# Kernel tuning notes

Measured on AMD Instinct MI355X. Metric: run time of the kernel, lower is better.

Reference implementation:

```python
import jax, jax.numpy as jnp
import numpy as np

B, D_IN, H, NZ, NC = 32768, 768, 2048, 128, 1024
EPS, NITERS = 0.5, 15


def setup_inputs() -> dict:
    key = jax.random.key(0)
    ks = jax.random.split(key, 4)
    x = jax.random.normal(ks[0], (B, D_IN), jnp.float32)
    # scaled init so feature magnitudes keep exp(-dist/eps) in f32 range
    W1 = jax.random.normal(ks[1], (D_IN, H), jnp.float32) / np.sqrt(D_IN)
    b1 = jnp.zeros((H,), jnp.float32)
    W2 = jax.random.normal(ks[2], (H, NZ), jnp.float32) / np.sqrt(H)
    b2 = jnp.zeros((NZ,), jnp.float32)
    centroids = jax.random.normal(ks[3], (NC, NZ), jnp.float32)
    return {
        'x': x, 'W1': W1, 'b1': b1, 'W2': W2, 'b2': b2,
        'centroids': centroids,
        'cluster_counts': jnp.zeros((NC,), jnp.int32),
        'raw_counts': jnp.zeros((NC,), jnp.int32),
        'total_soft_counts': jnp.zeros((NC,), jnp.float32),
    }


def _sinkhorn(scores, eps=EPS, niters=NITERS):
    # scores: [B, K].  Q: [K, B], matches torch reference where sum(Q) = col-sums.
    Q = jnp.exp(scores / eps).T
    Q = Q / jnp.sum(Q, axis=0, keepdims=True)
    K, Bb = Q.shape
    r = 1.0 / K
    c = 1.0 / Bb

    def body(Q, _):
        Q = Q * (r / jnp.sum(Q, axis=1))[:, None]
        Q = Q * (c / jnp.sum(Q, axis=0))[None, :]
        return Q, None

    Q, _ = jax.lax.scan(body, Q, None, length=niters)
    return (Q / jnp.sum(Q, axis=0, keepdims=True)).T  # [B, K]


def reference(x, W1, b1, W2, b2, centroids, cluster_counts, raw_counts, total_soft_counts):
    # fc backbone: Linear -> ReLU -> Linear
    fv = jax.nn.relu(x @ W1 + b1) @ W2 + b2                        # [B, nz]
    # pairwise euclidean distances to centroids (cdist via gram trick;
    # avoids materializing the [B, nc, nz] broadcast torch creates)
    sq = (jnp.sum(fv * fv, axis=1)[:, None]
          + jnp.sum(centroids * centroids, axis=1)[None, :]
          - 2.0 * fv @ centroids.T)
    cluster_dists = jnp.sqrt(jnp.maximum(sq, 1e-12))               # [B, nc]

    # sinkhorn branch (no_grad in torch)
    soft_assignments = jax.lax.stop_gradient(_sinkhorn(-cluster_dists))
    batch_assignments = jnp.argmin(soft_assignments, axis=1)       # [B]
    soft_counts = jnp.sum(soft_assignments, axis=0)                # [nc]
    # soft_train=False: gather assigned distances
    loss = jnp.mean(jnp.take_along_axis(cluster_dists, batch_assignments[:, None], axis=1))

    # scatter-accumulate counts
    new_raw = raw_counts.at[jnp.argmin(cluster_dists, axis=1)].add(1)
    new_cluster = cluster_counts.at[batch_assignments].add(1)
    new_total_soft = total_soft_counts + soft_counts
    return loss, batch_assignments, soft_counts, new_raw, new_cluster, new_total_soft
```

## Files before the change

kernel.cpp:

```cpp
#include <hip/hip_runtime.h>
#include <math.h>

#define BN    32768
#define DIN   768
#define HN    2048
#define NZ    128
#define NCN   1024

typedef __attribute__((ext_vector_type(8))) short s16x8;
typedef __attribute__((ext_vector_type(4))) float f32x4;
typedef unsigned short u16;

#define MFMA16(a,b,c) __builtin_amdgcn_mfma_f32_16x16x32_bf16(a,b,c,0,0,0)

__device__ __forceinline__ u16 bf16_rne(float x){
  unsigned u = __float_as_uint(x);
  unsigned r = (u + 0x7FFFu + ((u >> 16) & 1u)) >> 16;
  return (u16)r;
}
__device__ __forceinline__ float bf16_tof(u16 h){
  return __uint_as_float(((unsigned)h) << 16);
}
__device__ __forceinline__ void split3(float x, u16& h, u16& m, u16& l){
  h = bf16_rne(x);
  float r1 = x - bf16_tof(h);
  m = bf16_rne(r1);
  float r2 = r1 - bf16_tof(m);
  l = bf16_rne(r2);
}

__device__ __forceinline__ void gload16(const void* gsrc, void* lds){
  __builtin_amdgcn_global_load_lds(
      (const __attribute__((address_space(1))) unsigned int*)gsrc,
      (__attribute__((address_space(3))) unsigned int*)lds, 16, 0, 0);
}

__global__ __launch_bounds__(1024) void k0_init(float* u, int* hraw, int* hclu){
  const int k = threadIdx.x;
  u[k] = 1.0f;
  hraw[k] = 0;
  hclu[k] = 0;
}

__global__ __launch_bounds__(256) void c_tsplit(
    const float* __restrict__ in, int R, int C,
    u16* __restrict__ oh, u16* __restrict__ om, u16* __restrict__ ol)
{
  __shared__ float L[64][65];
  const int t = threadIdx.x;
  const int bi = blockIdx.x, bj = blockIdx.y;
  #pragma unroll
  for (int m=0;m<4;++m){
    int flat = t + 256*m;
    int r = flat >> 4, c4 = (flat & 15) << 2;
    const float4 v = *(const float4*)&in[(size_t)(bi*64 + r)*C + bj*64 + c4];
    L[r][c4+0] = v.x; L[r][c4+1] = v.y; L[r][c4+2] = v.z; L[r][c4+3] = v.w;
  }
  __syncthreads();
  #pragma unroll
  for (int m=0;m<4;++m){
    int flat = t + 256*m;
    int oc = flat >> 4, k4 = (flat & 15) << 2;
    ushort4 h4, m4, l4;
    split3(L[k4+0][oc], h4.x, m4.x, l4.x);
    split3(L[k4+1][oc], h4.y, m4.y, l4.y);
    split3(L[k4+2][oc], h4.z, m4.z, l4.z);
    split3(L[k4+3][oc], h4.w, m4.w, l4.w);
    size_t off = (size_t)(bj*64 + oc)*R + bi*64 + k4;
    *(ushort4*)&oh[off] = h4;
    *(ushort4*)&om[off] = m4;
    *(ushort4*)&ol[off] = l4;
  }
}

__global__ __launch_bounds__(256, 2) void k1_mfma(
    const float* __restrict__ X,
    const u16* __restrict__ W1h, const u16* __restrict__ W1m, const u16* __restrict__ W1l,
    const float* __restrict__ b1,
    const u16* __restrict__ W2h, const u16* __restrict__ W2m, const u16* __restrict__ W2l,
    const float* __restrict__ b2, float* __restrict__ fv)
{
  __shared__ __align__(16) unsigned char sm[73728];
  unsigned char* xsr = sm;
  unsigned char* wsr = sm + 24576;

  const int t  = threadIdx.x;
  const int l  = t & 63;
  const int wn = t >> 6;
  const int g  = (l >> 4) & 3;
  const int lr = l & 15;
  const int row0 = blockIdx.x * 64;

  f32x4 fvacc[4][2];
  #pragma unroll
  for (int mf=0;mf<4;++mf){
    fvacc[mf][0] = (f32x4){0.f,0.f,0.f,0.f};
    fvacc[mf][1] = (f32x4){0.f,0.f,0.f,0.f};
  }

  #pragma unroll 1
  for (int nc = 0; nc < 16; ++nc){
    f32x4 a1acc[4][2];
    #pragma unroll
    for (int mf=0;mf<4;++mf){
      a1acc[mf][0] = (f32x4){0.f,0.f,0.f,0.f};
      a1acc[mf][1] = (f32x4){0.f,0.f,0.f,0.f};
    }

    #pragma unroll 1
    for (int ks = 0; ks < 12; ++ks){
      #pragma unroll
      for (int m=0;m<4;++m){
        const int flat = t + 256*m;
        const int xr = flat >> 4;
        const int c4 = (flat & 15) << 2;
        f32x4 v = *(const f32x4*)&X[(size_t)(row0+xr)*768 + ks*64 + c4];
        ushort4 h4, m4, l4;
        split3(v[0], h4.x, m4.x, l4.x);
        split3(v[1], h4.y, m4.y, l4.y);
        split3(v[2], h4.z, m4.z, l4.z);
        split3(v[3], h4.w, m4.w, l4.w);
        const int bo = xr*128 + ((2*c4) ^ ((xr & 7) << 4));
        *(ushort4*)(xsr + bo)          = h4;
        *(ushort4*)(xsr + 8192 + bo)   = m4;
        *(ushort4*)(xsr + 16384 + bo)  = l4;
      }
      #pragma unroll
      for (int i=0;i<12;++i){
        const int ci = wn*12 + i;
        const int s  = ci >> 4;
        const int rb = ci & 15;
        const int rloc = rb*8 + (l >> 3);
        const int q  = l & 7;
        const u16* Wp = (s==0) ? W1h : ((s==1) ? W1m : W1l);
        const u16* src = Wp + (size_t)(nc*128 + rloc)*768 + ks*64 + ((q ^ (rloc & 7)) << 3);
        gload16(src, wsr + s*16384 + rb*1024);
      }
      __syncthreads();

      #pragma unroll
      for (int kk=0;kk<2;++kk){
        s16x8 Bf[3][2], Af[3][4];
        #pragma unroll
        for (int s=0;s<3;++s){
          #pragma unroll
          for (int nf=0;nf<2;++nf){
            const int br = wn*32 + nf*16 + lr;
            Bf[s][nf] = *(const s16x8*)(wsr + s*16384 + br*128 + ((16*(g + 4*kk)) ^ ((br & 7) << 4)));
          }
          #pragma unroll
          for (int mf=0;mf<4;++mf){
            const int ar = mf*16 + lr;
            Af[s][mf] = *(const s16x8*)(xsr + s*8192 + ar*128 + ((16*(g + 4*kk)) ^ ((ar & 7) << 4)));
          }
        }
        #pragma unroll
        for (int mf=0;mf<4;++mf){
          #pragma unroll
          for (int nf=0;nf<2;++nf){
            f32x4 acc = a1acc[mf][nf];
            acc = MFMA16(Af[0][mf], Bf[0][nf], acc);
            acc = MFMA16(Af[0][mf], Bf[1][nf], acc);
            acc = MFMA16(Af[1][mf], Bf[0][nf], acc);
            acc = MFMA16(Af[1][mf], Bf[1][nf], acc);
            acc = MFMA16(Af[0][mf], Bf[2][nf], acc);
            acc = MFMA16(Af[2][mf], Bf[0][nf], acc);
            a1acc[mf][nf] = acc;
          }
        }
      }
      __syncthreads();
    }

    const float b1v0 = b1[nc*128 + wn*32 + lr];
    const float b1v1 = b1[nc*128 + wn*32 + 16 + lr];

    #pragma unroll
    for (int half=0; half<2; ++half){
      if ((wn >> 1) == half){
        #pragma unroll
        for (int mf=0;mf<4;++mf){
          #pragma unroll
          for (int nf=0;nf<2;++nf){
            const int klocal = (wn & 1)*32 + nf*16 + lr;
            #pragma unroll
            for (int r=0;r<4;++r){
              float vv = a1acc[mf][nf][r] + ((nf==0) ? b1v0 : b1v1);
              vv = vv > 0.f ? vv : 0.f;
              u16 sh, sm2, sl;
              split3(vv, sh, sm2, sl);
              const int ar = mf*16 + g*4 + r;
              const int bo = ar*128 + ((2*klocal) ^ ((ar & 7) << 4));
              *(u16*)(xsr + bo)         = sh;
              *(u16*)(xsr + 8192 + bo)  = sm2;
              *(u16*)(xsr + 16384 + bo) = sl;
            }
          }
        }
      }
      #pragma unroll
      for (int i=0;i<12;++i){
        const int ci = wn*12 + i;
        const int s  = ci >> 4;
        const int rb = ci & 15;
        const int rloc = rb*8 + (l >> 3);
        const int q  = l & 7;
        const u16* Wp = (s==0) ? W2h : ((s==1) ? W2m : W2l);
        const u16* src = Wp + (size_t)rloc*2048 + nc*128 + half*64 + ((q ^ (rloc & 7)) << 3);
        gload16(src, wsr + s*16384 + rb*1024);
      }
      __syncthreads();

      #pragma unroll
      for (int kk=0;kk<2;++kk){
        s16x8 Bf[3][2], Af[3][4];
        #pragma unroll
        for (int s=0;s<3;++s){
          #pragma unroll
          for (int nf=0;nf<2;++nf){
            const int br = wn*32 + nf*16 + lr;
            Bf[s][nf] = *(const s16x8*)(wsr + s*16384 + br*128 + ((16*(g + 4*kk)) ^ ((br & 7) << 4)));
          }
          #pragma unroll
          for (int mf=0;mf<4;++mf){
            const int ar = mf*16 + lr;
            Af[s][mf] = *(const s16x8*)(xsr + s*8192 + ar*128 + ((16*(g + 4*kk)) ^ ((ar & 7) << 4)));
          }
        }
        #pragma unroll
        for (int mf=0;mf<4;++mf){
          #pragma unroll
          for (int nf=0;nf<2;++nf){
            f32x4 acc = fvacc[mf][nf];
            acc = MFMA16(Af[0][mf], Bf[0][nf], acc);
            acc = MFMA16(Af[0][mf], Bf[1][nf], acc);
            acc = MFMA16(Af[1][mf], Bf[0][nf], acc);
            acc = MFMA16(Af[1][mf], Bf[1][nf], acc);
            acc = MFMA16(Af[0][mf], Bf[2][nf], acc);
            acc = MFMA16(Af[2][mf], Bf[0][nf], acc);
            fvacc[mf][nf] = acc;
          }
        }
      }
      __syncthreads();
    }
  }

  const float b2v0 = b2[wn*32 + lr];
  const float b2v1 = b2[wn*32 + 16 + lr];
  #pragma unroll
  for (int mf=0;mf<4;++mf){
    #pragma unroll
    for (int nf=0;nf<2;++nf){
      #pragma unroll
      for (int r=0;r<4;++r){
        const int frow = row0 + mf*16 + g*4 + r;
        const int col  = wn*32 + nf*16 + lr;
        fv[(size_t)frow*NZ + col] = fvacc[mf][nf][r] + ((nf==0) ? b2v0 : b2v1);
      }
    }
  }
}

__global__ __launch_bounds__(256) void k2_dist(
    const float* __restrict__ fv, const float* __restrict__ cent,
    float* __restrict__ Q0)
{
  __shared__ __align__(16) float fvs[32*128];
  __shared__ __align__(16) float cs[64*128];
  __shared__ float fvn[32];
  __shared__ float cn[64];
  const int t = threadIdx.x;
  const int tx = t & 15, ty = t >> 4;
  const int row0 = blockIdx.x * 32;

  #pragma unroll
  for (int m=0;m<4;++m){
    int idx4 = t + 256*m;
    int r  = idx4 >> 5;
    int c4 = (idx4 & 31) << 2;
    *(float4*)&fvs[r*128 + (c4 ^ ((((r>>1)&7))<<2))] =
        *(const float4*)&fv[(size_t)(row0 + r)*NZ + c4];
  }
  __syncthreads();
  if (t < 32){
    int xw = ((t>>1)&7)<<2;
    float s = 0.f;
    for (int z=0;z<NZ;z+=4){
      const float4 v = *(const float4*)&fvs[t*128 + (z ^ xw)];
      s += v.x*v.x; s += v.y*v.y; s += v.z*v.z; s += v.w*v.w;
    }
    fvn[t] = s;
  }

  for (int cc = 0; cc < NCN; cc += 64){
    #pragma unroll
    for (int m=0;m<8;++m){
      int idx4 = t + 256*m;
      int r  = idx4 >> 5;
      int c4 = (idx4 & 31) << 2;
      *(float4*)&cs[r*128 + (c4 ^ ((((r>>3)&7))<<2))] =
          *(const float4*)&cent[(size_t)(cc + r)*NZ + c4];
    }
    __syncthreads();
    if (t < 64){
      int xw = ((t>>3)&7)<<2;
      float s = 0.f;
      for (int z=0;z<NZ;z+=4){
        const float4 v = *(const float4*)&cs[t*128 + (z ^ xw)];
        s += v.x*v.x; s += v.y*v.y; s += v.z*v.z; s += v.w*v.w;
      }
      cn[t] = s;
    }
    __syncthreads();

    float acc[2][4];
    #pragma unroll
    for (int i=0;i<2;++i)
      #pragma unroll
      for (int j=0;j<4;++j) acc[i][j]=0.f;

    const int xwf = (ty&7)<<2;
    const int xwc = ((tx>>1)&7)<<2;
    #pragma unroll 4
    for (int kk=0; kk<NZ; kk+=4){
      float4 fq0 = *(const float4*)&fvs[(2*ty+0)*128 + (kk ^ xwf)];
      float4 fq1 = *(const float4*)&fvs[(2*ty+1)*128 + (kk ^ xwf)];
      float4 cb[4];
      #pragma unroll
      for (int j=0;j<4;++j)
        cb[j] = *(const float4*)&cs[(4*tx+j)*128 + (kk ^ xwc)];
      #pragma unroll
      for (int j=0;j<4;++j){
        acc[0][j] += fq0.x*cb[j].x; acc[0][j] += fq0.y*cb[j].y;
        acc[0][j] += fq0.z*cb[j].z; acc[0][j] += fq0.w*cb[j].w;
        acc[1][j] += fq1.x*cb[j].x; acc[1][j] += fq1.y*cb[j].y;
        acc[1][j] += fq1.z*cb[j].z; acc[1][j] += fq1.w*cb[j].w;
      }
    }
    #pragma unroll
    for (int i=0;i<2;++i){
      int row = row0 + 2*ty + i;
      float fnv = fvn[2*ty+i];
      float o[4];
      #pragma unroll
      for (int j=0;j<4;++j){
        float sq = fnv + cn[4*tx+j] - 2.0f*acc[i][j];
        sq = sq > 1e-12f ? sq : 1e-12f;
        float d = sqrtf(sq);
        o[j] = expf(-2.0f*d);
      }
      float4 ov; ov.x=o[0]; ov.y=o[1]; ov.z=o[2]; ov.w=o[3];
      *(float4*)&Q0[(size_t)row*NCN + cc + 4*tx] = ov;
    }
    __syncthreads();
  }
}

__global__ __launch_bounds__(256) void k3_pass(
    const float* __restrict__ Q0, const float* __restrict__ u,
    float* __restrict__ S_part, float alpha)
{
  __shared__ __align__(16) float ul[NCN];
  __shared__ __align__(16) float Sw[4][NCN];
  const int t = threadIdx.x;
  const int w = t >> 6, l = t & 63;
  #pragma unroll
  for (int m=0;m<4;++m) ul[t + 256*m] = u[t + 256*m];
  #pragma unroll
  for (int m=0;m<16;++m) (&Sw[0][0])[t + 256*m] = 0.f;
  __syncthreads();

  const float4* ul4 = (const float4*)ul;
  float4* Sw4 = (float4*)&Sw[w][0];
  const int gw = blockIdx.x*4 + w;
  const size_t b0 = (size_t)gw * 16;
  for (int rr=0; rr<16; ++rr){
    const float4* qrow = (const float4*)(Q0 + (b0 + rr)*NCN);
    float4 q4[4];
    float part = 0.f;
    #pragma unroll
    for (int j=0;j<4;++j){
      q4[j] = qrow[l + 64*j];
      float4 uu = ul4[l + 64*j];
      part += q4[j].x*uu.x; part += q4[j].y*uu.y;
      part += q4[j].z*uu.z; part += q4[j].w*uu.w;
    }
    #pragma unroll
    for (int off=32; off; off>>=1) part += __shfl_xor(part, off, 64);
    const float v = alpha / part;
    #pragma unroll
    for (int j=0;j<4;++j){
      float4 s = Sw4[l + 64*j];
      s.x += q4[j].x*v; s.y += q4[j].y*v; s.z += q4[j].z*v; s.w += q4[j].w*v;
      Sw4[l + 64*j] = s;
    }
  }
  __syncthreads();
  #pragma unroll
  for (int m=0;m<4;++m){
    int k = t + 256*m;
    S_part[(size_t)blockIdx.x*NCN + k] = ((Sw[0][k]+Sw[1][k])+(Sw[2][k]+Sw[3][k]));
  }
}

__global__ __launch_bounds__(256) void k4_unew(
    const float* __restrict__ S_part, float* __restrict__ u)
{
  __shared__ float P[4][64];
  const int t = threadIdx.x;
  const int col = blockIdx.x*64 + (t & 63);
  const int s4 = t >> 6;
  float p = 0.f;
  for (int i=0;i<128;++i)
    p += S_part[(size_t)(s4*128 + i)*NCN + col];
  P[s4][t & 63] = p;
  __syncthreads();
  if (s4 == 0){
    float tot = ((P[0][t] + P[1][t]) + (P[2][t] + P[3][t]));
    u[col] = (1.0f/1024.0f) / tot;
  }
}

__device__ __forceinline__ float comp4(const float4 v, int c){
  return (c==0)?v.x:(c==1)?v.y:(c==2)?v.z:v.w;
}

__global__ __launch_bounds__(256) void k5_final(
    const float* __restrict__ Q0, const float* __restrict__ u,
    float* __restrict__ softc_part, float* __restrict__ loss_part,
    int* __restrict__ hist_raw, int* __restrict__ hist_clu,
    float* __restrict__ out_ba)
{
  __shared__ __align__(16) float ul[NCN];
  __shared__ __align__(16) float Sw[4][NCN];
  __shared__ float lossw[4];
  const int t = threadIdx.x;
  const int w = t >> 6, l = t & 63;
  #pragma unroll
  for (int m=0;m<4;++m) ul[t + 256*m] = u[t + 256*m];
  #pragma unroll
  for (int m=0;m<16;++m) (&Sw[0][0])[t + 256*m] = 0.f;
  __syncthreads();

  const float4* ul4 = (const float4*)ul;
  float4* Sw4 = (float4*)&Sw[w][0];
  const int gw = blockIdx.x*4 + w;
  const size_t b0 = (size_t)gw * 32;
  float lacc = 0.f;
  for (int rr=0; rr<32; ++rr){
    const size_t b = b0 + rr;
    const float4* qrow = (const float4*)(Q0 + b*NCN);
    float4 q4[4], wv4[4];
    float part = 0.f;
    #pragma unroll
    for (int j=0;j<4;++j){
      q4[j] = qrow[l + 64*j];
      float4 uu = ul4[l + 64*j];
      wv4[j].x = uu.x*q4[j].x; wv4[j].y = uu.y*q4[j].y;
      wv4[j].z = uu.z*q4[j].z; wv4[j].w = uu.w*q4[j].w;
      part += wv4[j].x; part += wv4[j].y; part += wv4[j].z; part += wv4[j].w;
    }
    #pragma unroll
    for (int off=32; off; off>>=1) part += __shfl_xor(part, off, 64);
    const float inv = 1.0f / part;

    float smin = wv4[0].x * inv; int kmin = 4*l; float qat = q4[0].x;
    float qmax = q4[0].x;        int kmax = 4*l;
    #pragma unroll
    for (int j=0;j<4;++j){
      #pragma unroll
      for (int c=0;c<4;++c){
        if (j==0 && c==0) continue;
        float qv = comp4(q4[j], c);
        float sv = comp4(wv4[j], c) * inv;
        int k = 4*l + 256*j + c;
        if (sv < smin){ smin = sv; kmin = k; qat = qv; }
        if (qv > qmax){ qmax = qv; kmax = k; }
      }
    }
    #pragma unroll
    for (int off=32; off; off>>=1){
      float s2 = __shfl_xor(smin, off, 64);
      int   k2 = __shfl_xor(kmin, off, 64);
      float q2 = __shfl_xor(qat,  off, 64);
      if (s2 < smin || (s2 == smin && k2 < kmin)){ smin=s2; kmin=k2; qat=q2; }
      float m2 = __shfl_xor(qmax, off, 64);
      int   i2 = __shfl_xor(kmax, off, 64);
      if (m2 > qmax || (m2 == qmax && i2 < kmax)){ qmax=m2; kmax=i2; }
    }
    #pragma unroll
    for (int j=0;j<4;++j){
      float4 s = Sw4[l + 64*j];
      s.x += wv4[j].x*inv; s.y += wv4[j].y*inv;
      s.z += wv4[j].z*inv; s.w += wv4[j].w*inv;
      Sw4[l + 64*j] = s;
    }
    if (l == 0){
      out_ba[b] = (float)kmin;
      atomicAdd(&hist_clu[kmin], 1);
      atomicAdd(&hist_raw[kmax], 1);
      lacc += -0.5f * logf(qat);
    }
  }
  if (l == 0) lossw[w] = lacc;
  __syncthreads();
  #pragma unroll
  for (int m=0;m<4;++m){
    int k = t + 256*m;
    softc_part[(size_t)blockIdx.x*NCN + k] = ((Sw[0][k]+Sw[1][k])+(Sw[2][k]+Sw[3][k]));
  }
  if (t == 0) loss_part[blockIdx.x] = ((lossw[0]+lossw[1])+(lossw[2]+lossw[3]));
}

__global__ __launch_bounds__(1024) void k6_fin(
    const float* __restrict__ softc_part, const float* __restrict__ loss_part,
    const int* __restrict__ hist_raw, const int* __restrict__ hist_clu,
    const int* __restrict__ raw_in, const int* __restrict__ clu_in,
    const float* __restrict__ tsoft_in, float* __restrict__ out)
{
  const int k = threadIdx.x;
  float s0=0.f,s1=0.f,s2=0.f,s3=0.f;
  for (int blk=0; blk<256; blk+=4){
    s0 += softc_part[(size_t)(blk+0)*NCN + k];
    s1 += softc_part[(size_t)(blk+1)*NCN + k];
    s2 += softc_part[(size_t)(blk+2)*NCN + k];
    s3 += softc_part[(size_t)(blk+3)*NCN + k];
  }
  const float s = ((s0+s1)+(s2+s3));
  out[1 + BN + k]           = s;
  out[1 + BN + NCN + k]     = (float)(raw_in[k] + hist_raw[k]);
  out[1 + BN + 2*NCN + k]   = (float)(clu_in[k] + hist_clu[k]);
  out[1 + BN + 3*NCN + k]   = tsoft_in[k] + s;
  if (k == 0){
    float ls = 0.f;
    for (int i=0;i<256;++i) ls += loss_part[i];
    out[0] = ls / 32768.0f;
  }
}

extern "C" void kernel_launch(void* const* d_in, const int* in_sizes, int n_in,
                              void* d_out, int out_size, void* d_ws, size_t ws_size,
                              hipStream_t stream) {
  (void)in_sizes; (void)n_in; (void)out_size; (void)ws_size;
  const float* x      = (const float*)d_in[0];
  const float* W1     = (const float*)d_in[1];
  const float* b1     = (const float*)d_in[2];
  const float* W2     = (const float*)d_in[3];
  const float* b2     = (const float*)d_in[4];
  const float* cent   = (const float*)d_in[5];
  const int*   clu_in = (const int*)d_in[6];
  const int*   raw_in = (const int*)d_in[7];
  const float* tsoft  = (const float*)d_in[8];
  float* out = (float*)d_out;

  float* ws        = (float*)d_ws;
  float* fv        = ws;
  float* Q0        = ws + 4194304;
  float* u         = Q0 + 33554432;
  float* S_part    = u + 1024;
  float* softc_par = S_part + 524288;
  float* loss_par  = softc_par + 262144;
  int*   hist_raw  = (int*)(loss_par + 256);
  int*   hist_clu  = hist_raw + 1024;
  u16* W1Th = (u16*)(ws + 38538496);
  u16* W1Tm = W1Th + 1572864;
  u16* W1Tl = W1Tm + 1572864;
  u16* W2Th = W1Tl + 1572864;
  u16* W2Tm = W2Th + 262144;
  u16* W2Tl = W2Tm + 262144;

  c_tsplit<<<dim3(12, 32), 256, 0, stream>>>(W1, 768, 2048, W1Th, W1Tm, W1Tl);
  c_tsplit<<<dim3(32, 2),  256, 0, stream>>>(W2, 2048, 128, W2Th, W2Tm, W2Tl);
  k0_init<<<1, 1024, 0, stream>>>(u, hist_raw, hist_clu);
  k1_mfma<<<512, 256, 0, stream>>>(x, W1Th, W1Tm, W1Tl, b1, W2Th, W2Tm, W2Tl, b2, fv);
  k2_dist<<<1024, 256, 0, stream>>>(fv, cent, Q0);
  for (int it = 0; it < 15; ++it){
    const float alpha = (it == 0) ? 1.0f : (1.0f/32768.0f);
    k3_pass<<<512, 256, 0, stream>>>(Q0, u, S_part, alpha);
    k4_unew<<<16, 256, 0, stream>>>(S_part, u);
  }
  k5_final<<<256, 256, 0, stream>>>(Q0, u, softc_par, loss_par,
                                    hist_raw, hist_clu, out + 1);
  k6_fin<<<1, 1024, 0, stream>>>(softc_par, loss_par, hist_raw, hist_clu,
                                 raw_in, clu_in, tsoft, out);
}
```

Baseline: 1.451 ms.

## Presplit X into bf16 triples and move distance GEMM to split-bf16 MFMA

Input X is split once into three bf16 planes by a separate kernel, so k1 loads its A tiles directly into LDS with global_load_lds instead of re-splitting X in every one of its 16 N-chunks. The fp32 FMA distance kernel is replaced by a 6-term split-bf16 MFMA kernel, with fv and centroid norms precomputed by separate small kernels. This removes redundant conversion work and the scalar-FMA bottleneck, but adds extra HBM traffic for the split X (three u16 planes written then read) and several extra launches. Workspace buffers are aliased (X planes share Q0's space, fv and centroid planes share the weight planes' space).

```diff
diff --git a/kernel.cpp b/kernel.cpp
--- a/kernel.cpp
+++ b/kernel.cpp
@@ -40,6 +40,23 @@
   u[k] = 1.0f;
   hraw[k] = 0;
   hclu[k] = 0;
+}
+
+__global__ __launch_bounds__(256) void c_split(
+    const float* __restrict__ in, u16* __restrict__ oh, u16* __restrict__ om,
+    u16* __restrict__ ol, int n4)
+{
+  const int i = blockIdx.x*256 + threadIdx.x;
+  if (i >= n4) return;
+  const f32x4 v = *(const f32x4*)&in[(size_t)i*4];
+  ushort4 h4, m4, l4;
+  split3(v[0], h4.x, m4.x, l4.x);
+  split3(v[1], h4.y, m4.y, l4.y);
+  split3(v[2], h4.z, m4.z, l4.z);
+  split3(v[3], h4.w, m4.w, l4.w);
+  *(ushort4*)&oh[(size_t)i*4] = h4;
+  *(ushort4*)&om[(size_t)i*4] = m4;
+  *(ushort4*)&ol[(size_t)i*4] = l4;
 }
 
 __global__ __launch_bounds__(256) void c_tsplit(
@@ -73,8 +90,20 @@
   }
 }
 
+__global__ __launch_bounds__(256) void c_norm(
+    const float* __restrict__ in, float* __restrict__ out)
+{
+  const int w = threadIdx.x >> 6, l = threadIdx.x & 63;
+  const int row = blockIdx.x*4 + w;
+  const float2 v = *(const float2*)&in[(size_t)row*128 + l*2];
+  float s = v.x*v.x + v.y*v.y;
+  #pragma unroll
+  for (int off=32; off; off>>=1) s += __shfl_xor(s, off, 64);
+  if (l == 0) out[row] = s;
+}
+
 __global__ __launch_bounds__(256, 2) void k1_mfma(
-    const float* __restrict__ X,
+    const u16* __restrict__ Xh, const u16* __restrict__ Xm, const u16* __restrict__ Xl,
     const u16* __restrict__ W1h, const u16* __restrict__ W1m, const u16* __restrict__ W1l,
     const float* __restrict__ b1,
     const u16* __restrict__ W2h, const u16* __restrict__ W2m, const u16* __restrict__ W2l,
@@ -110,20 +139,15 @@
     #pragma unroll 1
     for (int ks = 0; ks < 12; ++ks){
       #pragma unroll
-      for (int m=0;m<4;++m){
-        const int flat = t + 256*m;
-        const int xr = flat >> 4;
-        const int c4 = (flat & 15) << 2;
-        f32x4 v = *(const f32x4*)&X[(size_t)(row0+xr)*768 + ks*64 + c4];
-        ushort4 h4, m4, l4;
-        split3(v[0], h4.x, m4.x, l4.x);
-        split3(v[1], h4.y, m4.y, l4.y);
-        split3(v[2], h4.z, m4.z, l4.z);
-        split3(v[3], h4.w, m4.w, l4.w);
-        const int bo = xr*128 + ((2*c4) ^ ((xr & 7) << 4));
-        *(ushort4*)(xsr + bo)          = h4;
-        *(ushort4*)(xsr + 8192 + bo)   = m4;
-        *(ushort4*)(xsr + 16384 + bo)  = l4;
+      for (int i=0;i<6;++i){
+        const int ci = wn*6 + i;
+        const int s  = ci >> 3;
+        const int rb = ci & 7;
+        const int xr = rb*8 + (l >> 3);
+        const int q  = l & 7;
+        const u16* Xp = (s==0) ? Xh : ((s==1) ? Xm : Xl);
+        const u16* src = Xp + (size_t)(row0 + xr)*768 + ks*64 + ((q ^ (xr & 7)) << 3);
+        gload16(src, xsr + s*8192 + rb*1024);
       }
       #pragma unroll
       for (int i=0;i<12;++i){
@@ -262,96 +286,88 @@
   }
 }
 
-__global__ __launch_bounds__(256) void k2_dist(
-    const float* __restrict__ fv, const float* __restrict__ cent,
+__global__ __launch_bounds__(256, 2) void k2_mfma(
+    const u16* __restrict__ fvh, const u16* __restrict__ fvm, const u16* __restrict__ fvl,
+    const u16* __restrict__ ch,  const u16* __restrict__ cm,  const u16* __restrict__ cl,
+    const float* __restrict__ fvn, const float* __restrict__ cn,
     float* __restrict__ Q0)
 {
-  __shared__ __align__(16) float fvs[32*128];
-  __shared__ __align__(16) float cs[64*128];
-  __shared__ float fvn[32];
-  __shared__ float cn[64];
-  const int t = threadIdx.x;
-  const int tx = t & 15, ty = t >> 4;
-  const int row0 = blockIdx.x * 32;
-
-  #pragma unroll
-  for (int m=0;m<4;++m){
-    int idx4 = t + 256*m;
-    int r  = idx4 >> 5;
-    int c4 = (idx4 & 31) << 2;
-    *(float4*)&fvs[r*128 + (c4 ^ ((((r>>1)&7))<<2))] =
-        *(const float4*)&fv[(size_t)(row0 + r)*NZ + c4];
-  }
-  __syncthreads();
-  if (t < 32){
-    int xw = ((t>>1)&7)<<2;
-    float s = 0.f;
-    for (int z=0;z<NZ;z+=4){
-      const float4 v = *(const float4*)&fvs[t*128 + (z ^ xw)];
-      s += v.x*v.x; s += v.y*v.y; s += v.z*v.z; s += v.w*v.w;
-    }
-    fvn[t] = s;
-  }
-
+  __shared__ __align__(16) unsigned char bs[49152];
+  __shared__ float cnl[NCN];
+  const int t  = threadIdx.x;
+  const int l  = t & 63;
+  const int wn = t >> 6;
+  const int g  = (l >> 4) & 3;
+  const int lr = l & 15;
+  const int row0 = blockIdx.x * 64;
+  const int arow = row0 + wn*16 + lr;
+
+  s16x8 Af[3][4];
+  #pragma unroll
+  for (int kk=0;kk<4;++kk){
+    const size_t ao = (size_t)arow*128 + kk*32 + g*8;
+    Af[0][kk] = *(const s16x8*)&fvh[ao];
+    Af[1][kk] = *(const s16x8*)&fvm[ao];
+    Af[2][kk] = *(const s16x8*)&fvl[ao];
+  }
+  #pragma unroll
+  for (int m=0;m<4;++m) cnl[t + 256*m] = cn[t + 256*m];
+  const f32x4 fvnv = *(const f32x4*)&fvn[row0 + wn*16 + g*4];
+
+  #pragma unroll 1
   for (int cc = 0; cc < NCN; cc += 64){
     #pragma unroll
-    for (int m=0;m<8;++m){
-      int idx4 = t + 256*m;
-      int r  = idx4 >> 5;
-      int c4 = (idx4 & 31) << 2;
-      *(float4*)&cs[r*128 + (c4 ^ ((((r>>3)&7))<<2))] =
-          *(const float4*)&cent[(size_t)(cc + r)*NZ + c4];
+    for (int i=0;i<12;++i){
+      const int ci = wn*12 + i;
+      const int s  = ci >> 4;
+      const int rb = ci & 15;
+      const int crow = rb*4 + (l >> 4);
+      const int q  = l & 15;
+      const u16* Cp = (s==0) ? ch : ((s==1) ? cm : cl);
+      const u16* src = Cp + (size_t)(cc + crow)*128 + ((q ^ (crow & 15)) << 3);
+      gload16(src, bs + s*16384 + rb*1024);
     }
     __syncthreads();
-    if (t < 64){
-      int xw = ((t>>3)&7)<<2;
-      float s = 0.f;
-      for (int z=0;z<NZ;z+=4){
-        const float4 v = *(const float4*)&cs[t*128 + (z ^ xw)];
-        s += v.x*v.x; s += v.y*v.y; s += v.z*v.z; s += v.w*v.w;
-      }
-      cn[t] = s;
-    }
-    __syncthreads();
-
-    float acc[2][4];
-    #pragma unroll
-    for (int i=0;i<2;++i)
-      #pragma unroll
-      for (int j=0;j<4;++j) acc[i][j]=0.f;
-
-    const int xwf = (ty&7)<<2;
-    const int xwc = ((tx>>1)&7)<<2;
-    #pragma unroll 4
-    for (int kk=0; kk<NZ; kk+=4){
-      float4 fq0 = *(const float4*)&fvs[(2*ty+0)*128 + (kk ^ xwf)];
-      float4 fq1 = *(const float4*)&fvs[(2*ty+1)*128 + (kk ^ xwf)];
-      float4 cb[4];
-      #pragma unroll
-      for (int j=0;j<4;++j)
-        cb[j] = *(const float4*)&cs[(4*tx+j)*128 + (kk ^ xwc)];
-      #pragma unroll
-      for (int j=0;j<4;++j){
-        acc[0][j] += fq0.x*cb[j].x; acc[0][j] += fq0.y*cb[j].y;
-        acc[0][j] += fq0.z*cb[j].z; acc[0][j] += fq0.w*cb[j].w;
-        acc[1][j] += fq1.x*cb[j].x; acc[1][j] += fq1.y*cb[j].y;
-        acc[1][j] += fq1.z*cb[j].z; acc[1][j] += fq1.w*cb[j].w;
-      }
-    }
-    #pragma unroll
-    for (int i=0;i<2;++i){
-      int row = row0 + 2*ty + i;
-      float fnv = fvn[2*ty+i];
-      float o[4];
-      #pragma unroll
-      for (int j=0;j<4;++j){
-        float sq = fnv + cn[4*tx+j] - 2.0f*acc[i][j];
+
+    f32x4 acc[4];
+    #pragma unroll
+    for (int nf=0;nf<4;++nf) acc[nf] = (f32x4){0.f,0.f,0.f,0.f};
+
+    #pragma unroll
+    for (int kk=0;kk<4;++kk){
+      s16x8 Bq[3][4];
+      #pragma unroll
+      for (int nf=0;nf<4;++nf){
+        const int br = nf*16 + lr;
+        const int base = br*256 + (((g + 4*kk) ^ (br & 15)) << 4);
+        Bq[0][nf] = *(const s16x8*)(bs + base);
+        Bq[1][nf] = *(const s16x8*)(bs + 16384 + base);
+        Bq[2][nf] = *(const s16x8*)(bs + 32768 + base);
+      }
+      #pragma unroll
+      for (int nf=0;nf<4;++nf){
+        f32x4 a = acc[nf];
+        a = MFMA16(Af[0][kk], Bq[0][nf], a);
+        a = MFMA16(Af[0][kk], Bq[1][nf], a);
+        a = MFMA16(Af[1][kk], Bq[0][nf], a);
+        a = MFMA16(Af[1][kk], Bq[1][nf], a);
+        a = MFMA16(Af[0][kk], Bq[2][nf], a);
+        a = MFMA16(Af[2][kk], Bq[0][nf], a);
+        acc[nf] = a;
+      }
+    }
+
+    #pragma unroll
+    for (int nf=0;nf<4;++nf){
+      const int n = cc + nf*16 + lr;
+      const float cv = cnl[n];
+      #pragma unroll
+      for (int r=0;r<4;++r){
+        float sq = fvnv[r] + cv - 2.0f*acc[nf][r];
         sq = sq > 1e-12f ? sq : 1e-12f;
-        float d = sqrtf(sq);
-        o[j] = expf(-2.0f*d);
-      }
-      float4 ov; ov.x=o[0]; ov.y=o[1]; ov.z=o[2]; ov.w=o[3];
-      *(float4*)&Q0[(size_t)row*NCN + cc + 4*tx] = ov;
+        const float d = sqrtf(sq);
+        Q0[(size_t)(row0 + wn*16 + g*4 + r)*NCN + n] = expf(-2.0f*d);
+      }
     }
     __syncthreads();
   }
@@ -557,24 +573,46 @@
   float* ws        = (float*)d_ws;
   float* fv        = ws;
   float* Q0        = ws + 4194304;
-  float* u         = Q0 + 33554432;
+  u16*   Xh        = (u16*)Q0;
+  u16*   Xm        = Xh + 25165824;
+  u16*   Xl        = Xm + 25165824;
+  float* u         = ws + 41943040;
   float* S_part    = u + 1024;
   float* softc_par = S_part + 524288;
   float* loss_par  = softc_par + 262144;
   int*   hist_raw  = (int*)(loss_par + 256);
   int*   hist_clu  = hist_raw + 1024;
-  u16* W1Th = (u16*)(ws + 38538496);
+  float* wbase     = (float*)(hist_clu + 1024);
+  u16* W1Th = (u16*)wbase;
   u16* W1Tm = W1Th + 1572864;
   u16* W1Tl = W1Tm + 1572864;
   u16* W2Th = W1Tl + 1572864;
   u16* W2Tm = W2Th + 262144;
   u16* W2Tl = W2Tm + 262144;
-
+  u16* fvh = (u16*)wbase;
+  u16* fvm = fvh + 4194304;
+  u16* fvl = fvm + 4194304;
+  u16* ch  = fvl + 4194304;
+  u16* cm  = ch  + 131072;
+  u16* cl  = cm  + 131072;
+  float* fvn = wbase + 6488064;
+  float* cn  = fvn + 32768;
+
+  c_split <<<24576, 256, 0, stream>>>(x, Xh, Xm, Xl, 6291456);
   c_tsplit<<<dim3(12, 32), 256, 0, stream>>>(W1, 768, 2048, W1Th, W1Tm, W1Tl);
   c_tsplit<<<dim3(32, 2),  256, 0, stream>>>(W2, 2048, 128, W2Th, W2Tm, W2Tl);
   k0_init<<<1, 1024, 0, stream>>>(u, hist_raw, hist_clu);
-  k1_mfma<<<512, 256, 0, stream>>>(x, W1Th, W1Tm, W1Tl, b1, W2Th, W2Tm, W2Tl, b2, fv);
-  k2_dist<<<1024, 256, 0, stream>>>(fv, cent, Q0);
+
+  k1_mfma<<<512, 256, 0, stream>>>(Xh, Xm, Xl, W1Th, W1Tm, W1Tl, b1,
+                                   W2Th, W2Tm, W2Tl, b2, fv);
+
+  c_split<<<4096, 256, 0, stream>>>(fv,   fvh, fvm, fvl, 1048576);
+  c_split<<<128,  256, 0, stream>>>(cent, ch,  cm,  cl,  32768);
+  c_norm <<<8192, 256, 0, stream>>>(fv,   fvn);
+  c_norm <<<256,  256, 0, stream>>>(cent, cn);
+
+  k2_mfma<<<512, 256, 0, stream>>>(fvh, fvm, fvl, ch, cm, cl, fvn, cn, Q0);
+
   for (int it = 0; it < 15; ++it){
     const float alpha = (it == 0) ? 1.0f : (1.0f/32768.0f);
     k3_pass<<<512, 256, 0, stream>>>(Q0, u, S_part, alpha);
```

Measured after the change: 1.317 ms. -9.2%, faster.
